# Kernel tuning notes

Hardware: AMD Instinct MI355X
Metric: run time of the kernel (lower is better)

Reference implementation:

```python
import jax, jax.numpy as jnp
import numpy as np

BN_EPS = 1e-5

def _conv(x, W, b, stride, pad):
    # x: [B,C,H,W], W: [O,I,kh,kw]
    y = jax.lax.conv_general_dilated(
        x, W, window_strides=(stride, stride),
        padding=[(pad, pad), (pad, pad)],
        dimension_numbers=('NCHW', 'OIHW', 'NCHW'))
    return y + b[None, :, None, None]

def _bn(x, gamma, beta, mean, var):
    inv = gamma * jax.lax.rsqrt(var + BN_EPS)
    return x * inv[None, :, None, None] + (beta - mean * inv)[None, :, None, None]

def _haar_cD(x):
    # pywt.dwt2(x, 'haar') diagonal detail over last two axes (even H,W):
    # cD[i,j] = (x[2i,2j] - x[2i,2j+1] - x[2i+1,2j] + x[2i+1,2j+1]) / 2
    a = x[..., 0::2, 0::2]
    b = x[..., 0::2, 1::2]
    c = x[..., 1::2, 0::2]
    d = x[..., 1::2, 1::2]
    return (a - b - c + d) * 0.5

def setup_inputs() -> dict:
    key = jax.random.key(0)
    ks = jax.random.split(key, 20)
    B = 8192
    f32 = jnp.float32
    inp = {
        'x':   jax.random.normal(ks[0], (B, 3, 32, 32), dtype=f32),
        # conv1: 3 -> 32, k5 s2 p2
        'w1':  jax.random.normal(ks[1], (32, 3, 5, 5), dtype=f32) * 0.05,
        'b1':  jnp.zeros((32,), f32),
        'g1':  jnp.ones((32,), f32),
        'be1': jnp.zeros((32,), f32),
        'm1':  jax.random.normal(ks[2], (32,), dtype=f32) * 0.1,
        'v1':  jax.random.uniform(ks[3], (32,), dtype=f32, minval=0.5, maxval=1.5),
        # conv2: 32 -> 64, k3 s2 p1
        'w2':  jax.random.normal(ks[4], (64, 32, 3, 3), dtype=f32) * 0.05,
        'b2':  jnp.zeros((64,), f32),
        'g2':  jnp.ones((64,), f32),
        'be2': jnp.zeros((64,), f32),
        'm2':  jax.random.normal(ks[5], (64,), dtype=f32) * 0.1,
        'v2':  jax.random.uniform(ks[6], (64,), dtype=f32, minval=0.5, maxval=1.5),
        # attention conv: 64 -> 1, k1
        'wa':  jax.random.normal(ks[7], (1, 64, 1, 1), dtype=f32) * 0.1,
        'ba':  jnp.zeros((1,), f32),
        # decoder linears (torch Linear layout: [out, in])
        'wd1': jax.random.normal(ks[8], (512, 64 * 8 * 8), dtype=f32) * 0.02,
        'bd1': jnp.zeros((512,), f32),
        'wd2': jax.random.normal(ks[9], (128, 512), dtype=f32) * 0.04,
        'bd2': jnp.zeros((128,), f32),
    }
    return inp

def reference(x, w1, b1, g1, be1, m1, v1, w2, b2, g2, be2, m2, v2,
              wa, ba, wd1, bd1, wd2, bd2):
    # wavelet_conv stem
    h = jax.nn.relu(_bn(_conv(x, w1, b1, 2, 2), g1, be1, m1, v1))   # [B,32,16,16]
    feat = jax.nn.relu(_bn(_conv(h, w2, b2, 2, 1), g2, be2, m2, v2))  # [B,64,8,8]
    # Haar DWT diagonal-detail gate (detached in the original)
    cD = jax.lax.stop_gradient(_haar_cD(feat))                        # [B,64,4,4]
    cD_up = jnp.repeat(jnp.repeat(cD, 2, axis=-2), 2, axis=-1)        # [B,64,8,8]
    feat = feat * cD_up
    # attention gate
    attn = jax.nn.sigmoid(_conv(feat, wa, ba, 1, 0))                  # [B,1,8,8]
    feat = feat * attn
    # decode
    f = feat.reshape(feat.shape[0], -1)                               # [B,4096]
    h1 = jax.nn.relu(f @ wd1.T + bd1)                                  # [B,512]
    return jax.nn.sigmoid(h1 @ wd2.T + bd2)                            # [B,128]
```

## Files before the change

### kernel.cpp

```cpp
#include <hip/hip_runtime.h>
#include <hip/hip_bf16.h>

typedef __bf16 bf16x8 __attribute__((ext_vector_type(8)));
typedef __bf16 bf16x4 __attribute__((ext_vector_type(4)));
typedef float f32x4 __attribute__((ext_vector_type(4)));

#define BN_EPS 1e-5f

__device__ __forceinline__ void gl_lds16(const __bf16* g, __bf16* l) {
    __builtin_amdgcn_global_load_lds(
        (const __attribute__((address_space(1))) unsigned int*)g,
        (__attribute__((address_space(3))) unsigned int*)l,
        16, 0, 0);
}

__global__ __launch_bounds__(256) void wd1p_kernel(const float* __restrict__ wd1, __bf16* __restrict__ o) {
    __shared__ float t2[64][65];
    const int n = blockIdx.x;
    const int tid = threadIdx.x;
    const float* src = wd1 + (size_t)n * 4096;
    #pragma unroll
    for (int r = 0; r < 16; ++r) {
        int j = r * 256 + tid;
        t2[j & 63][j >> 6] = src[j];
    }
    __syncthreads();
    __bf16* dst = o + (size_t)n * 4096;
    #pragma unroll
    for (int r = 0; r < 16; ++r) {
        int t = r * 256 + tid;
        dst[t] = (__bf16)t2[t >> 6][t & 63];
    }
}

__global__ void prep_kernel(const float* __restrict__ wd2, const float* __restrict__ w1,
                            const float* __restrict__ w2,
                            __bf16* __restrict__ wd2o, __bf16* __restrict__ w1o,
                            __bf16* __restrict__ w2o) {
    int i = blockIdx.x * 256 + threadIdx.x;
    if (i < 65536) { wd2o[i] = (__bf16)wd2[i]; return; }
    i -= 65536;
    if (i < 4096) {
        int oc = i >> 7, rem = i & 127;
        int ot = rem >> 3, j = rem & 7;
        float v = 0.f;
        if (ot < 15 && j < 5) {
            int ic = ot / 5, ky = ot % 5;
            v = w1[((oc * 3 + ic) * 5 + ky) * 5 + j];
        }
        w1o[i] = (__bf16)v;
        return;
    }
    i -= 4096;
    if (i < 18432) {
        int oc = i / 288, rem = i % 288;
        int tap = rem / 32, ic = rem % 32;
        w2o[i] = (__bf16)w2[(oc * 32 + ic) * 9 + tap];
    }
}

__global__ __launch_bounds__(256, 5) void conv_fused_kernel(
    const float* __restrict__ x,
    const __bf16* __restrict__ w1r, const float* __restrict__ b1,
    const float* __restrict__ g1, const float* __restrict__ be1,
    const float* __restrict__ m1, const float* __restrict__ v1,
    const __bf16* __restrict__ w2r, const float* __restrict__ b2,
    const float* __restrict__ g2, const float* __restrict__ be2,
    const float* __restrict__ m2, const float* __restrict__ v2,
    const float* __restrict__ wa, const float* __restrict__ ba,
    __bf16* __restrict__ f)
{
    __shared__ __align__(16) __bf16 xsb[3 * 36 * 40];
    __shared__ __align__(16) char  ubuf[23552];
    __bf16* hsf  = (__bf16*)ubuf;
    float*  feat = (float*)ubuf;
    float*  cds  = (float*)(ubuf + 17408);
    float*  atn  = (float*)(ubuf + 22528);

    const int b    = blockIdx.x;
    const int tid  = threadIdx.x;
    const int lane = tid & 63;
    const int wave = tid >> 6;
    const int lo   = lane >> 4;
    const int ln   = lane & 15;

    {
        bf16x8 z = {};
        for (int i = tid; i < 540; i += 256) *(bf16x8*)&xsb[i * 8] = z;
        if (tid < 132) {
            int pi = tid >> 2, ch = tid & 3;
            int pix = (pi < 17) ? pi : (pi - 16) * 17;
            *(bf16x8*)&hsf[pix * 40 + ch * 8] = z;
        }
    }
    __syncthreads();

    {
        const float4* xb = (const float4*)(x + (size_t)b * 3072);
        #pragma unroll
        for (int r = 0; r < 3; ++r) {
            int c = r * 256 + tid;
            int plane = c >> 8, rem = c & 255;
            int row = rem >> 3, c4 = rem & 7;
            float4 v = xb[c];
            bf16x4 h;
            h[0] = (__bf16)v.x; h[1] = (__bf16)v.y; h[2] = (__bf16)v.z; h[3] = (__bf16)v.w;
            *(bf16x4*)&xsb[plane * 1440 + (row + 2) * 40 + 4 + c4 * 4] = h;
        }
    }

    bf16x8 bw1[2][4];
    #pragma unroll
    for (int nt = 0; nt < 2; ++nt)
        #pragma unroll
        for (int s = 0; s < 4; ++s)
            bw1[nt][s] = *(const bf16x8*)(w1r + (nt * 16 + ln) * 128 + (s * 4 + lo) * 8);
    __syncthreads();

    f32x4 c1[4][2] = {};
    const unsigned int* xw = (const unsigned int*)xsb;
    #pragma unroll
    for (int s = 0; s < 4; ++s) {
        const int o  = s * 4 + lo;
        const int ic = (o * 205) >> 10;
        const int ky = o - ic * 5;
        const bool dummy = (o == 15);
        const int icc = dummy ? 2 : ic;
        #pragma unroll
        for (int mt = 0; mt < 4; ++mt) {
            const int oy  = wave * 4 + mt;
            const int row = dummy ? 35 : (2 * oy + ky);
            const int dw  = icc * 720 + row * 20 + ln + 1;
            union { unsigned int u[4]; bf16x8 v; } fa;
            fa.u[0] = xw[dw]; fa.u[1] = xw[dw + 1]; fa.u[2] = xw[dw + 2]; fa.u[3] = 0;
            #pragma unroll
            for (int nt = 0; nt < 2; ++nt)
                c1[mt][nt] = __builtin_amdgcn_mfma_f32_16x16x32_bf16(fa.v, bw1[nt][s], c1[mt][nt], 0, 0, 0);
        }
    }

    #pragma unroll
    for (int nt = 0; nt < 2; ++nt) {
        const int oc  = nt * 16 + ln;
        const float inv = g1[oc] * rsqrtf(v1[oc] + BN_EPS);
        const float bb  = be1[oc] + (b1[oc] - m1[oc]) * inv;
        #pragma unroll
        for (int mt = 0; mt < 4; ++mt) {
            const int hy = wave * 4 + mt + 1;
            #pragma unroll
            for (int r = 0; r < 4; ++r) {
                const int hx = lo * 4 + r + 1;
                hsf[(hy * 17 + hx) * 40 + oc] = (__bf16)fmaxf(c1[mt][nt][r] * inv + bb, 0.f);
            }
        }
    }

    const int wm = wave >> 1, wn = wave & 1;
    bf16x8 bw2[2][9];
    #pragma unroll
    for (int nt = 0; nt < 2; ++nt) {
        const __bf16* wp = w2r + (wn * 32 + nt * 16 + ln) * 288 + lo * 8;
        #pragma unroll
        for (int ks = 0; ks < 9; ++ks)
            bw2[nt][ks] = *(const bf16x8*)(wp + ks * 32);
    }
    __syncthreads();

    f32x4 c2[2][2] = {};
    {
        int pixbase[2];
        #pragma unroll
        for (int mt = 0; mt < 2; ++mt) {
            int p = wm * 32 + mt * 16 + ln;
            int qy = p >> 3, qx = p & 7;
            pixbase[mt] = (2 * qy * 17 + 2 * qx) * 40 + lo * 8;
        }
        #pragma unroll
        for (int ks = 0; ks < 9; ++ks) {
            const int ty = ks / 3, tx = ks % 3;
            bf16x8 af[2];
            #pragma unroll
            for (int mt = 0; mt < 2; ++mt)
                af[mt] = *(const bf16x8*)&hsf[pixbase[mt] + (ty * 17 + tx) * 40];
            #pragma unroll
            for (int mt = 0; mt < 2; ++mt)
                #pragma unroll
                for (int nt = 0; nt < 2; ++nt)
                    c2[mt][nt] = __builtin_amdgcn_mfma_f32_16x16x32_bf16(af[mt], bw2[nt][ks], c2[mt][nt], 0, 0, 0);
        }
    }
    __syncthreads();

    #pragma unroll
    for (int nt = 0; nt < 2; ++nt) {
        const int oc  = wn * 32 + nt * 16 + ln;
        const float inv = g2[oc] * rsqrtf(v2[oc] + BN_EPS);
        const float bb  = be2[oc] + (b2[oc] - m2[oc]) * inv;
        #pragma unroll
        for (int mt = 0; mt < 2; ++mt) {
            const int p0 = wm * 32 + mt * 16 + lo * 4;
            f32x4 o;
            #pragma unroll
            for (int r = 0; r < 4; ++r)
                o[r] = fmaxf(c2[mt][nt][r] * inv + bb, 0.f);
            *(f32x4*)&feat[oc * 68 + p0] = o;
        }
    }
    __syncthreads();

    {
        const int c = tid >> 2, y = tid & 3;
        const float* fr = feat + c * 68 + 16 * y;
        f32x4 t0 = *(const f32x4*)(fr);
        f32x4 t2 = *(const f32x4*)(fr + 4);
        f32x4 t1 = *(const f32x4*)(fr + 8);
        f32x4 t3 = *(const f32x4*)(fr + 12);
        f32x4 o;
        o[0] = 0.5f * (t0[0] - t0[1] - t1[0] + t1[1]);
        o[1] = 0.5f * (t0[2] - t0[3] - t1[2] + t1[3]);
        o[2] = 0.5f * (t2[0] - t2[1] - t3[0] + t3[1]);
        o[3] = 0.5f * (t2[2] - t2[3] - t3[2] + t3[3]);
        *(f32x4*)&cds[c * 20 + y * 4] = o;
    }
    __syncthreads();

    const int q  = tid & 63;
    const int g  = wave;
    const int qy2 = q >> 3, qx2 = q & 7;
    const int qq = (qy2 >> 1) * 4 + (qx2 >> 1);
    float a2[16];
    float part = 0.f;
    #pragma unroll
    for (int j = 0; j < 16; ++j) {
        int oc = g * 16 + j;
        float v = feat[oc * 68 + q] * cds[oc * 20 + qq];
        a2[j] = v;
        part += v * wa[oc];
    }
    atn[g * 64 + q] = part;
    __syncthreads();
    float s2  = atn[q] + atn[64 + q] + atn[128 + q] + atn[192 + q] + ba[0];
    float sig = 1.f / (1.f + __expf(-s2));

    bf16x8 fo0, fo1;
    #pragma unroll
    for (int j = 0; j < 8; ++j) {
        fo0[j] = (__bf16)(a2[j] * sig);
        fo1[j] = (__bf16)(a2[j + 8] * sig);
    }
    __bf16* fb = f + (size_t)b * 4096 + q * 64 + g * 16;
    *(bf16x8*)fb = fo0;
    *(bf16x8*)(fb + 8) = fo1;
}

__global__ __launch_bounds__(256, 4) void gemm1_split_kernel(
    const __bf16* __restrict__ A, const __bf16* __restrict__ B,
    float* __restrict__ P)
{
    const int K = 4096, NOUT = 512, KH = 2048;
    __shared__ __align__(16) __bf16 As[64][64];
    __shared__ __align__(16) __bf16 Bs[128][64];
    const int tid  = threadIdx.x;
    const int lane = tid & 63;
    const int wave = tid >> 6;
    const int lo = lane >> 4, ln = lane & 15;
    const int bid = blockIdx.x;
    const int swz = (bid & 7) * 128 + (bid >> 3);
    const int n0  = (swz & 3) * 128;
    const int zz  = (swz >> 2) & 1;
    const int m0  = (swz >> 3) * 64;
    const int ks0 = zz * KH;
    const int sw = ln & 7;
    f32x4 acc[4][2] = {};
    for (int k0 = ks0; k0 < ks0 + KH; k0 += 64) {
        #pragma unroll
        for (int r = 0; r < 2; ++r) {
            int i = r * 256 + tid;
            int row = i >> 3, cs = i & 7;
            gl_lds16(A + (size_t)(m0 + row) * K + k0 + (cs ^ (row & 7)) * 8, &As[0][0] + i * 8);
        }
        #pragma unroll
        for (int r = 0; r < 4; ++r) {
            int i = r * 256 + tid;
            int row = i >> 3, cs = i & 7;
            gl_lds16(B + (size_t)(n0 + row) * K + k0 + (cs ^ (row & 7)) * 8, &Bs[0][0] + i * 8);
        }
        __syncthreads();
        #pragma unroll
        for (int s = 0; s < 2; ++s) {
            const int c = s * 4 + lo;
            const int slot = (c ^ sw) * 8;
            bf16x8 af[4], bfr[2];
            #pragma unroll
            for (int mt = 0; mt < 4; ++mt)
                af[mt] = *(const bf16x8*)(&As[mt * 16 + ln][slot]);
            #pragma unroll
            for (int nt = 0; nt < 2; ++nt)
                bfr[nt] = *(const bf16x8*)(&Bs[wave * 32 + nt * 16 + ln][slot]);
            #pragma unroll
            for (int mt = 0; mt < 4; ++mt)
                #pragma unroll
                for (int nt = 0; nt < 2; ++nt)
                    acc[mt][nt] = __builtin_amdgcn_mfma_f32_16x16x32_bf16(af[mt], bfr[nt], acc[mt][nt], 0, 0, 0);
        }
        __syncthreads();
    }
    float* Pp = P + (size_t)zz * 8192 * 512;
    #pragma unroll
    for (int mt = 0; mt < 4; ++mt)
        #pragma unroll
        for (int nt = 0; nt < 2; ++nt)
            #pragma unroll
            for (int r = 0; r < 4; ++r) {
                int m = m0 + mt * 16 + lo * 4 + r;
                int n = n0 + wave * 32 + nt * 16 + ln;
                Pp[(size_t)m * NOUT + n] = acc[mt][nt][r];
            }
}

__global__ __launch_bounds__(256) void reduce1_kernel(
    const float* __restrict__ P, const float* __restrict__ bias, __bf16* __restrict__ h1)
{
    const size_t HALF = (size_t)8192 * 512;
    size_t i4 = ((size_t)blockIdx.x * 256 + threadIdx.x) * 4;
    f32x4 p0 = *(const f32x4*)(P + i4);
    f32x4 p1 = *(const f32x4*)(P + HALF + i4);
    f32x4 bv = *(const f32x4*)(bias + (i4 & 511));
    bf16x4 o;
    #pragma unroll
    for (int j = 0; j < 4; ++j)
        o[j] = (__bf16)fmaxf(p0[j] + p1[j] + bv[j], 0.f);
    *(bf16x4*)(h1 + i4) = o;
}

__global__ __launch_bounds__(256) void gemm1_kernel(
    const __bf16* __restrict__ A, const __bf16* __restrict__ B,
    const float* __restrict__ bias, __bf16* __restrict__ C)
{
    const int K = 4096, NOUT = 512;
    __shared__ __align__(16) __bf16 As[64][64];
    __shared__ __align__(16) __bf16 Bs[128][64];
    const int tid  = threadIdx.x;
    const int lane = tid & 63;
    const int wave = tid >> 6;
    const int lo = lane >> 4, ln = lane & 15;
    const int bid = blockIdx.x;
    const int swz = (bid & 7) * 64 + (bid >> 3);
    const int n0  = (swz & 3) * 128;
    const int m0  = (swz >> 2) * 64;
    const int sw = ln & 7;
    f32x4 acc[4][2] = {};
    for (int k0 = 0; k0 < K; k0 += 64) {
        #pragma unroll
        for (int r = 0; r < 2; ++r) {
            int i = r * 256 + tid;
            int row = i >> 3, cs = i & 7;
            gl_lds16(A + (size_t)(m0 + row) * K + k0 + (cs ^ (row & 7)) * 8, &As[0][0] + i * 8);
        }
        #pragma unroll
        for (int r = 0; r < 4; ++r) {
            int i = r * 256 + tid;
            int row = i >> 3, cs = i & 7;
            gl_lds16(B + (size_t)(n0 + row) * K + k0 + (cs ^ (row & 7)) * 8, &Bs[0][0] + i * 8);
        }
        __syncthreads();
        #pragma unroll
        for (int s = 0; s < 2; ++s) {
            const int c = s * 4 + lo;
            const int slot = (c ^ sw) * 8;
            bf16x8 af[4], bfr[2];
            #pragma unroll
            for (int mt = 0; mt < 4; ++mt)
                af[mt] = *(const bf16x8*)(&As[mt * 16 + ln][slot]);
            #pragma unroll
            for (int nt = 0; nt < 2; ++nt)
                bfr[nt] = *(const bf16x8*)(&Bs[wave * 32 + nt * 16 + ln][slot]);
            #pragma unroll
            for (int mt = 0; mt < 4; ++mt)
                #pragma unroll
                for (int nt = 0; nt < 2; ++nt)
                    acc[mt][nt] = __builtin_amdgcn_mfma_f32_16x16x32_bf16(af[mt], bfr[nt], acc[mt][nt], 0, 0, 0);
        }
        __syncthreads();
    }
    #pragma unroll
    for (int mt = 0; mt < 4; ++mt)
        #pragma unroll
        for (int nt = 0; nt < 2; ++nt)
            #pragma unroll
            for (int r = 0; r < 4; ++r) {
                int m = m0 + mt * 16 + lo * 4 + r;
                int n = n0 + wave * 32 + nt * 16 + ln;
                float v = acc[mt][nt][r] + bias[n];
                C[(size_t)m * NOUT + n] = (__bf16)fmaxf(v, 0.f);
            }
}

__global__ __launch_bounds__(256, 4) void gemm2_kernel(
    const __bf16* __restrict__ A, const __bf16* __restrict__ B,
    const float* __restrict__ bias, float* __restrict__ Out)
{
    const int K = 512, NOUT = 128;
    __shared__ __align__(16) __bf16 As[32][64];
    __shared__ __align__(16) __bf16 Bs[128][64];
    const int tid  = threadIdx.x;
    const int lane = tid & 63;
    const int wave = tid >> 6;
    const int lo = lane >> 4, ln = lane & 15;
    const int m0 = blockIdx.x * 32;
    const int sw = ln & 7;
    f32x4 acc[2][2] = {};
    for (int k0 = 0; k0 < K; k0 += 64) {
        {
            int i = tid;
            int row = i >> 3, cs = i & 7;
            gl_lds16(A + (size_t)(m0 + row) * K + k0 + (cs ^ (row & 7)) * 8, &As[0][0] + i * 8);
        }
        #pragma unroll
        for (int r = 0; r < 4; ++r) {
            int i = r * 256 + tid;
            int row = i >> 3, cs = i & 7;
            gl_lds16(B + (size_t)row * K + k0 + (cs ^ (row & 7)) * 8, &Bs[0][0] + i * 8);
        }
        __syncthreads();
        #pragma unroll
        for (int s = 0; s < 2; ++s) {
            const int c = s * 4 + lo;
            const int slot = (c ^ sw) * 8;
            bf16x8 af[2], bfr[2];
            #pragma unroll
            for (int mt = 0; mt < 2; ++mt)
                af[mt] = *(const bf16x8*)(&As[mt * 16 + ln][slot]);
            #pragma unroll
            for (int nt = 0; nt < 2; ++nt)
                bfr[nt] = *(const bf16x8*)(&Bs[wave * 32 + nt * 16 + ln][slot]);
            #pragma unroll
            for (int mt = 0; mt < 2; ++mt)
                #pragma unroll
                for (int nt = 0; nt < 2; ++nt)
                    acc[mt][nt] = __builtin_amdgcn_mfma_f32_16x16x32_bf16(af[mt], bfr[nt], acc[mt][nt], 0, 0, 0);
        }
        __syncthreads();
    }
    #pragma unroll
    for (int mt = 0; mt < 2; ++mt)
        #pragma unroll
        for (int nt = 0; nt < 2; ++nt)
            #pragma unroll
            for (int r = 0; r < 4; ++r) {
                int m = m0 + mt * 16 + lo * 4 + r;
                int n = wave * 32 + nt * 16 + ln;
                float v = acc[mt][nt][r] + bias[n];
                Out[(size_t)m * NOUT + n] = 1.f / (1.f + __expf(-v));
            }
}

extern "C" void kernel_launch(void* const* d_in, const int* in_sizes, int n_in,
                              void* d_out, int out_size, void* d_ws, size_t ws_size,
                              hipStream_t stream)
{
    const float* x   = (const float*)d_in[0];
    const float* w1  = (const float*)d_in[1];
    const float* b1  = (const float*)d_in[2];
    const float* g1  = (const float*)d_in[3];
    const float* be1 = (const float*)d_in[4];
    const float* m1  = (const float*)d_in[5];
    const float* v1  = (const float*)d_in[6];
    const float* w2  = (const float*)d_in[7];
    const float* b2  = (const float*)d_in[8];
    const float* g2  = (const float*)d_in[9];
    const float* be2 = (const float*)d_in[10];
    const float* m2  = (const float*)d_in[11];
    const float* v2  = (const float*)d_in[12];
    const float* wa  = (const float*)d_in[13];
    const float* ba  = (const float*)d_in[14];
    const float* wd1 = (const float*)d_in[15];
    const float* bd1 = (const float*)d_in[16];
    const float* wd2 = (const float*)d_in[17];
    const float* bd2 = (const float*)d_in[18];

    char* ws = (char*)d_ws;
    const size_t SZ_F  = 67108864;
    const size_t SZ_P  = 33554432;
    const size_t SZ_H1 = 8388608;
    const bool use_split = ws_size >= (SZ_F + SZ_P + SZ_H1 + 4194304 + 131072 + 65536 + 8192);

    __bf16* f_bf = (__bf16*)ws;
    float*  P;
    __bf16* h1_bf;
    char* tail;
    if (use_split) {
        P      = (float*)(ws + SZ_F);
        h1_bf  = (__bf16*)(ws + SZ_F + SZ_P);
        tail   = ws + SZ_F + SZ_P + SZ_H1;
    } else {
        P      = nullptr;
        h1_bf  = (__bf16*)(ws + SZ_F);
        tail   = ws + SZ_F + SZ_H1;
    }
    __bf16* wd1_bf = (__bf16*)tail;
    __bf16* wd2_bf = (__bf16*)(tail + 4194304);
    __bf16* w2r_bf = (__bf16*)(tail + 4194304 + 131072);
    __bf16* w1r_bf = (__bf16*)(tail + 4194304 + 131072 + 65536);

    prep_kernel<<<344, 256, 0, stream>>>(wd2, w1, w2, wd2_bf, w1r_bf, w2r_bf);
    wd1p_kernel<<<512, 256, 0, stream>>>(wd1, wd1_bf);

    conv_fused_kernel<<<8192, 256, 0, stream>>>(x, w1r_bf, b1, g1, be1, m1, v1,
                                                w2r_bf, b2, g2, be2, m2, v2, wa, ba, f_bf);

    if (use_split) {
        gemm1_split_kernel<<<1024, 256, 0, stream>>>(f_bf, wd1_bf, P);
        reduce1_kernel<<<4096, 256, 0, stream>>>(P, bd1, h1_bf);
    } else {
        gemm1_kernel<<<512, 256, 0, stream>>>(f_bf, wd1_bf, bd1, h1_bf);
    }

    gemm2_kernel<<<256, 256, 0, stream>>>(h1_bf, wd2_bf, bd2, (float*)d_out);
}
```

Before: 308.1 us.

## Widen conv block to 512 threads and use 128x128 split-K gemm1 tiles

The fused conv kernel now runs 512 threads per image: each wave owns half as many rows and output channels, and weight fragments are loaded per step instead of held in registers. The aim is to cut register pressure and raise occupancy. The first linear layer's split-K gemm grows from a 64x128 to a 128x128 tile per block and can split K four ways when workspace allows, with the reduce kernel summing a variable number of partials. This brings more data reuse per block and more parallel blocks, at the cost of extra partial-sum traffic and lower gemm occupancy.

```diff
diff --git a/kernel.cpp b/kernel.cpp
--- a/kernel.cpp
+++ b/kernel.cpp
@@ -4,6 +4,7 @@
 typedef __bf16 bf16x8 __attribute__((ext_vector_type(8)));
 typedef __bf16 bf16x4 __attribute__((ext_vector_type(4)));
 typedef float f32x4 __attribute__((ext_vector_type(4)));
+typedef float f32x2 __attribute__((ext_vector_type(2)));
 
 #define BN_EPS 1e-5f
 
@@ -59,7 +60,7 @@
     }
 }
 
-__global__ __launch_bounds__(256, 5) void conv_fused_kernel(
+__global__ __launch_bounds__(512, 8) void conv_fused_kernel(
     const float* __restrict__ x,
     const __bf16* __restrict__ w1r, const float* __restrict__ b1,
     const float* __restrict__ g1, const float* __restrict__ be1,
@@ -71,7 +72,7 @@
     __bf16* __restrict__ f)
 {
     __shared__ __align__(16) __bf16 xsb[3 * 36 * 40];
-    __shared__ __align__(16) char  ubuf[23552];
+    __shared__ __align__(16) char  ubuf[24576];
     __bf16* hsf  = (__bf16*)ubuf;
     float*  feat = (float*)ubuf;
     float*  cds  = (float*)(ubuf + 17408);
@@ -86,7 +87,7 @@
 
     {
         bf16x8 z = {};
-        for (int i = tid; i < 540; i += 256) *(bf16x8*)&xsb[i * 8] = z;
+        for (int i = tid; i < 540; i += 512) *(bf16x8*)&xsb[i * 8] = z;
         if (tid < 132) {
             int pi = tid >> 2, ch = tid & 3;
             int pix = (pi < 17) ? pi : (pi - 16) * 17;
@@ -98,44 +99,43 @@
     {
         const float4* xb = (const float4*)(x + (size_t)b * 3072);
         #pragma unroll
-        for (int r = 0; r < 3; ++r) {
-            int c = r * 256 + tid;
-            int plane = c >> 8, rem = c & 255;
-            int row = rem >> 3, c4 = rem & 7;
-            float4 v = xb[c];
-            bf16x4 h;
-            h[0] = (__bf16)v.x; h[1] = (__bf16)v.y; h[2] = (__bf16)v.z; h[3] = (__bf16)v.w;
-            *(bf16x4*)&xsb[plane * 1440 + (row + 2) * 40 + 4 + c4 * 4] = h;
-        }
-    }
-
-    bf16x8 bw1[2][4];
-    #pragma unroll
-    for (int nt = 0; nt < 2; ++nt)
-        #pragma unroll
-        for (int s = 0; s < 4; ++s)
-            bw1[nt][s] = *(const bf16x8*)(w1r + (nt * 16 + ln) * 128 + (s * 4 + lo) * 8);
-    __syncthreads();
-
-    f32x4 c1[4][2] = {};
+        for (int r = 0; r < 2; ++r) {
+            int c = r * 512 + tid;
+            if (c < 768) {
+                int plane = c >> 8, rem = c & 255;
+                int row = rem >> 3, c4 = rem & 7;
+                float4 v = xb[c];
+                bf16x4 h;
+                h[0] = (__bf16)v.x; h[1] = (__bf16)v.y; h[2] = (__bf16)v.z; h[3] = (__bf16)v.w;
+                *(bf16x4*)&xsb[plane * 1440 + (row + 2) * 40 + 4 + c4 * 4] = h;
+            }
+        }
+    }
+    __syncthreads();
+
+    f32x4 c1[2][2] = {};
     const unsigned int* xw = (const unsigned int*)xsb;
-    #pragma unroll
+    #pragma unroll 1
     for (int s = 0; s < 4; ++s) {
+        bf16x8 bw1s[2];
+        #pragma unroll
+        for (int nt = 0; nt < 2; ++nt)
+            bw1s[nt] = *(const bf16x8*)(w1r + (nt * 16 + ln) * 128 + (s * 4 + lo) * 8);
         const int o  = s * 4 + lo;
         const int ic = (o * 205) >> 10;
         const int ky = o - ic * 5;
         const bool dummy = (o == 15);
         const int icc = dummy ? 2 : ic;
         #pragma unroll
-        for (int mt = 0; mt < 4; ++mt) {
-            const int oy  = wave * 4 + mt;
+        for (int mt = 0; mt < 2; ++mt) {
+            const int oy  = wave * 2 + mt;
             const int row = dummy ? 35 : (2 * oy + ky);
             const int dw  = icc * 720 + row * 20 + ln + 1;
             union { unsigned int u[4]; bf16x8 v; } fa;
             fa.u[0] = xw[dw]; fa.u[1] = xw[dw + 1]; fa.u[2] = xw[dw + 2]; fa.u[3] = 0;
             #pragma unroll
             for (int nt = 0; nt < 2; ++nt)
-                c1[mt][nt] = __builtin_amdgcn_mfma_f32_16x16x32_bf16(fa.v, bw1[nt][s], c1[mt][nt], 0, 0, 0);
+                c1[mt][nt] = __builtin_amdgcn_mfma_f32_16x16x32_bf16(fa.v, bw1s[nt], c1[mt][nt], 0, 0, 0);
         }
     }
 
@@ -145,8 +145,8 @@
         const float inv = g1[oc] * rsqrtf(v1[oc] + BN_EPS);
         const float bb  = be1[oc] + (b1[oc] - m1[oc]) * inv;
         #pragma unroll
-        for (int mt = 0; mt < 4; ++mt) {
-            const int hy = wave * 4 + mt + 1;
+        for (int mt = 0; mt < 2; ++mt) {
+            const int hy = wave * 2 + mt + 1;
             #pragma unroll
             for (int r = 0; r < 4; ++r) {
                 const int hx = lo * 4 + r + 1;
@@ -154,19 +154,10 @@
             }
         }
     }
-
-    const int wm = wave >> 1, wn = wave & 1;
-    bf16x8 bw2[2][9];
-    #pragma unroll
-    for (int nt = 0; nt < 2; ++nt) {
-        const __bf16* wp = w2r + (wn * 32 + nt * 16 + ln) * 288 + lo * 8;
-        #pragma unroll
-        for (int ks = 0; ks < 9; ++ks)
-            bw2[nt][ks] = *(const bf16x8*)(wp + ks * 32);
-    }
-    __syncthreads();
-
-    f32x4 c2[2][2] = {};
+    __syncthreads();
+
+    const int wm = wave >> 2, wn = wave & 3;
+    f32x4 c2[2] = {};
     {
         int pixbase[2];
         #pragma unroll
@@ -175,25 +166,23 @@
             int qy = p >> 3, qx = p & 7;
             pixbase[mt] = (2 * qy * 17 + 2 * qx) * 40 + lo * 8;
         }
-        #pragma unroll
+        const __bf16* wp = w2r + (wn * 16 + ln) * 288 + lo * 8;
+        #pragma unroll 1
         for (int ks = 0; ks < 9; ++ks) {
+            bf16x8 bw2s = *(const bf16x8*)(wp + ks * 32);
             const int ty = ks / 3, tx = ks % 3;
-            bf16x8 af[2];
-            #pragma unroll
-            for (int mt = 0; mt < 2; ++mt)
-                af[mt] = *(const bf16x8*)&hsf[pixbase[mt] + (ty * 17 + tx) * 40];
-            #pragma unroll
-            for (int mt = 0; mt < 2; ++mt)
-                #pragma unroll
-                for (int nt = 0; nt < 2; ++nt)
-                    c2[mt][nt] = __builtin_amdgcn_mfma_f32_16x16x32_bf16(af[mt], bw2[nt][ks], c2[mt][nt], 0, 0, 0);
-        }
-    }
-    __syncthreads();
-
-    #pragma unroll
-    for (int nt = 0; nt < 2; ++nt) {
-        const int oc  = wn * 32 + nt * 16 + ln;
+            const int off = (ty * 17 + tx) * 40;
+            #pragma unroll
+            for (int mt = 0; mt < 2; ++mt) {
+                bf16x8 af = *(const bf16x8*)&hsf[pixbase[mt] + off];
+                c2[mt] = __builtin_amdgcn_mfma_f32_16x16x32_bf16(af, bw2s, c2[mt], 0, 0, 0);
+            }
+        }
+    }
+    __syncthreads();
+
+    {
+        const int oc  = wn * 16 + ln;
         const float inv = g2[oc] * rsqrtf(v2[oc] + BN_EPS);
         const float bb  = be2[oc] + (b2[oc] - m2[oc]) * inv;
         #pragma unroll
@@ -202,79 +191,75 @@
             f32x4 o;
             #pragma unroll
             for (int r = 0; r < 4; ++r)
-                o[r] = fmaxf(c2[mt][nt][r] * inv + bb, 0.f);
+                o[r] = fmaxf(c2[mt][r] * inv + bb, 0.f);
             *(f32x4*)&feat[oc * 68 + p0] = o;
         }
     }
     __syncthreads();
 
     {
-        const int c = tid >> 2, y = tid & 3;
-        const float* fr = feat + c * 68 + 16 * y;
+        const int c = tid >> 3, y = (tid >> 1) & 3, h = tid & 1;
+        const float* fr = feat + c * 68 + 16 * y + 4 * h;
         f32x4 t0 = *(const f32x4*)(fr);
-        f32x4 t2 = *(const f32x4*)(fr + 4);
         f32x4 t1 = *(const f32x4*)(fr + 8);
-        f32x4 t3 = *(const f32x4*)(fr + 12);
-        f32x4 o;
+        f32x2 o;
         o[0] = 0.5f * (t0[0] - t0[1] - t1[0] + t1[1]);
         o[1] = 0.5f * (t0[2] - t0[3] - t1[2] + t1[3]);
-        o[2] = 0.5f * (t2[0] - t2[1] - t3[0] + t3[1]);
-        o[3] = 0.5f * (t2[2] - t2[3] - t3[2] + t3[3]);
-        *(f32x4*)&cds[c * 20 + y * 4] = o;
-    }
-    __syncthreads();
-
-    const int q  = tid & 63;
+        *(f32x2*)&cds[c * 20 + y * 4 + 2 * h] = o;
+    }
+    __syncthreads();
+
+    const int q  = lane;
     const int g  = wave;
     const int qy2 = q >> 3, qx2 = q & 7;
     const int qq = (qy2 >> 1) * 4 + (qx2 >> 1);
-    float a2[16];
+    float a2[8];
     float part = 0.f;
     #pragma unroll
-    for (int j = 0; j < 16; ++j) {
-        int oc = g * 16 + j;
+    for (int j = 0; j < 8; ++j) {
+        int oc = g * 8 + j;
         float v = feat[oc * 68 + q] * cds[oc * 20 + qq];
         a2[j] = v;
         part += v * wa[oc];
     }
     atn[g * 64 + q] = part;
     __syncthreads();
-    float s2  = atn[q] + atn[64 + q] + atn[128 + q] + atn[192 + q] + ba[0];
+    float s2 = ba[0];
+    #pragma unroll
+    for (int k = 0; k < 8; ++k) s2 += atn[k * 64 + q];
     float sig = 1.f / (1.f + __expf(-s2));
 
-    bf16x8 fo0, fo1;
-    #pragma unroll
-    for (int j = 0; j < 8; ++j) {
-        fo0[j] = (__bf16)(a2[j] * sig);
-        fo1[j] = (__bf16)(a2[j + 8] * sig);
-    }
-    __bf16* fb = f + (size_t)b * 4096 + q * 64 + g * 16;
-    *(bf16x8*)fb = fo0;
-    *(bf16x8*)(fb + 8) = fo1;
-}
-
-__global__ __launch_bounds__(256, 4) void gemm1_split_kernel(
+    bf16x8 fo;
+    #pragma unroll
+    for (int j = 0; j < 8; ++j)
+        fo[j] = (__bf16)(a2[j] * sig);
+    *(bf16x8*)(f + (size_t)b * 4096 + q * 64 + g * 8) = fo;
+}
+
+__global__ __launch_bounds__(256, 3) void gemm1_split_kernel(
     const __bf16* __restrict__ A, const __bf16* __restrict__ B,
-    float* __restrict__ P)
+    float* __restrict__ P, int zlog, int chunk)
 {
-    const int K = 4096, NOUT = 512, KH = 2048;
-    __shared__ __align__(16) __bf16 As[64][64];
+    const int K = 4096, NOUT = 512;
+    const int KH = K >> zlog;
+    __shared__ __align__(16) __bf16 As[128][64];
     __shared__ __align__(16) __bf16 Bs[128][64];
     const int tid  = threadIdx.x;
     const int lane = tid & 63;
     const int wave = tid >> 6;
     const int lo = lane >> 4, ln = lane & 15;
+    const int wm = wave >> 1, wn = wave & 1;
     const int bid = blockIdx.x;
-    const int swz = (bid & 7) * 128 + (bid >> 3);
+    const int swz = (bid & 7) * chunk + (bid >> 3);
     const int n0  = (swz & 3) * 128;
-    const int zz  = (swz >> 2) & 1;
-    const int m0  = (swz >> 3) * 64;
+    const int zz  = (swz >> 2) & ((1 << zlog) - 1);
+    const int m0  = (swz >> (2 + zlog)) * 128;
     const int ks0 = zz * KH;
-    const int sw = ln & 7;
-    f32x4 acc[4][2] = {};
+    const int sw  = ln & 7;
+    f32x4 acc[4][4] = {};
     for (int k0 = ks0; k0 < ks0 + KH; k0 += 64) {
         #pragma unroll
-        for (int r = 0; r < 2; ++r) {
+        for (int r = 0; r < 4; ++r) {
             int i = r * 256 + tid;
             int row = i >> 3, cs = i & 7;
             gl_lds16(A + (size_t)(m0 + row) * K + k0 + (cs ^ (row & 7)) * 8, &As[0][0] + i * 8);
@@ -290,17 +275,17 @@
         for (int s = 0; s < 2; ++s) {
             const int c = s * 4 + lo;
             const int slot = (c ^ sw) * 8;
-            bf16x8 af[4], bfr[2];
+            bf16x8 af[4], bfr[4];
             #pragma unroll
             for (int mt = 0; mt < 4; ++mt)
-                af[mt] = *(const bf16x8*)(&As[mt * 16 + ln][slot]);
-            #pragma unroll
-            for (int nt = 0; nt < 2; ++nt)
-                bfr[nt] = *(const bf16x8*)(&Bs[wave * 32 + nt * 16 + ln][slot]);
+                af[mt] = *(const bf16x8*)(&As[wm * 64 + mt * 16 + ln][slot]);
+            #pragma unroll
+            for (int nt = 0; nt < 4; ++nt)
+                bfr[nt] = *(const bf16x8*)(&Bs[wn * 64 + nt * 16 + ln][slot]);
             #pragma unroll
             for (int mt = 0; mt < 4; ++mt)
                 #pragma unroll
-                for (int nt = 0; nt < 2; ++nt)
+                for (int nt = 0; nt < 4; ++nt)
                     acc[mt][nt] = __builtin_amdgcn_mfma_f32_16x16x32_bf16(af[mt], bfr[nt], acc[mt][nt], 0, 0, 0);
         }
         __syncthreads();
@@ -309,27 +294,29 @@
     #pragma unroll
     for (int mt = 0; mt < 4; ++mt)
         #pragma unroll
-        for (int nt = 0; nt < 2; ++nt)
+        for (int nt = 0; nt < 4; ++nt)
             #pragma unroll
             for (int r = 0; r < 4; ++r) {
-                int m = m0 + mt * 16 + lo * 4 + r;
-                int n = n0 + wave * 32 + nt * 16 + ln;
+                int m = m0 + wm * 64 + mt * 16 + lo * 4 + r;
+                int n = n0 + wn * 64 + nt * 16 + ln;
                 Pp[(size_t)m * NOUT + n] = acc[mt][nt][r];
             }
 }
 
 __global__ __launch_bounds__(256) void reduce1_kernel(
-    const float* __restrict__ P, const float* __restrict__ bias, __bf16* __restrict__ h1)
+    const float* __restrict__ P, const float* __restrict__ bias, __bf16* __restrict__ h1,
+    int nz)
 {
-    const size_t HALF = (size_t)8192 * 512;
+    const size_t Q = (size_t)8192 * 512;
     size_t i4 = ((size_t)blockIdx.x * 256 + threadIdx.x) * 4;
-    f32x4 p0 = *(const f32x4*)(P + i4);
-    f32x4 p1 = *(const f32x4*)(P + HALF + i4);
+    f32x4 s = *(const f32x4*)(P + i4);
+    for (int z = 1; z < nz; ++z)
+        s += *(const f32x4*)(P + (size_t)z * Q + i4);
     f32x4 bv = *(const f32x4*)(bias + (i4 & 511));
     bf16x4 o;
     #pragma unroll
     for (int j = 0; j < 4; ++j)
-        o[j] = (__bf16)fmaxf(p0[j] + p1[j] + bv[j], 0.f);
+        o[j] = (__bf16)fmaxf(s[j] + bv[j], 0.f);
     *(bf16x4*)(h1 + i4) = o;
 }
 
@@ -480,16 +467,21 @@
     const float* bd2 = (const float*)d_in[18];
 
     char* ws = (char*)d_ws;
-    const size_t SZ_F  = 67108864;
-    const size_t SZ_P  = 33554432;
-    const size_t SZ_H1 = 8388608;
-    const bool use_split = ws_size >= (SZ_F + SZ_P + SZ_H1 + 4194304 + 131072 + 65536 + 8192);
+    const size_t SZ_F   = 67108864;
+    const size_t SZ_H1  = 8388608;
+    const size_t SZ_P1  = 16777216;
+    const size_t TAILSZ = 4194304 + 131072 + 65536 + 8192;
+
+    int nz = 0;
+    if      (ws_size >= SZ_F + 4 * SZ_P1 + SZ_H1 + TAILSZ) nz = 4;
+    else if (ws_size >= SZ_F + 2 * SZ_P1 + SZ_H1 + TAILSZ) nz = 2;
 
     __bf16* f_bf = (__bf16*)ws;
     float*  P;
     __bf16* h1_bf;
     char* tail;
-    if (use_split) {
+    if (nz) {
+        size_t SZ_P = (size_t)nz * SZ_P1;
         P      = (float*)(ws + SZ_F);
         h1_bf  = (__bf16*)(ws + SZ_F + SZ_P);
         tail   = ws + SZ_F + SZ_P + SZ_H1;
@@ -506,12 +498,14 @@
     prep_kernel<<<344, 256, 0, stream>>>(wd2, w1, w2, wd2_bf, w1r_bf, w2r_bf);
     wd1p_kernel<<<512, 256, 0, stream>>>(wd1, wd1_bf);
 
-    conv_fused_kernel<<<8192, 256, 0, stream>>>(x, w1r_bf, b1, g1, be1, m1, v1,
+    conv_fused_kernel<<<8192, 512, 0, stream>>>(x, w1r_bf, b1, g1, be1, m1, v1,
                                                 w2r_bf, b2, g2, be2, m2, v2, wa, ba, f_bf);
 
-    if (use_split) {
-        gemm1_split_kernel<<<1024, 256, 0, stream>>>(f_bf, wd1_bf, P);
-        reduce1_kernel<<<4096, 256, 0, stream>>>(P, bd1, h1_bf);
+    if (nz) {
+        const int zlog = (nz == 4) ? 2 : 1;
+        const int blocks = 256 * nz;
+        gemm1_split_kernel<<<blocks, 256, 0, stream>>>(f_bf, wd1_bf, P, zlog, blocks >> 3);
+        reduce1_kernel<<<4096, 256, 0, stream>>>(P, bd1, h1_bf, nz);
     } else {
         gemm1_kernel<<<512, 256, 0, stream>>>(f_bf, wd1_bf, bd1, h1_bf);
     }
```

Measured after the change: 353.8 us. +14.8%, slower.

## Fuse split-K reduction into gemm2 and process two images per conv block

Applied to the files above, without the earlier changes.

Removes the separate reduce1 kernel: when split-K is used, gemm2 loads both fp32 partial sums, adds the bias, applies ReLU and converts to bf16 directly into its LDS A tile. This drops one launch and the h1 write/read round trip. The conv kernel now runs 512-thread blocks that each handle two images with duplicated shared buffers, which halves the number of blocks. The trade-offs are a synchronous load path in place of async global_load_lds, and a different occupancy profile with 2 blocks per CU.

```diff
diff --git a/kernel.cpp b/kernel.cpp
--- a/kernel.cpp
+++ b/kernel.cpp
@@ -59,7 +59,7 @@
     }
 }
 
-__global__ __launch_bounds__(256, 5) void conv_fused_kernel(
+__global__ __launch_bounds__(512, 2) void conv_fused_kernel(
     const float* __restrict__ x,
     const __bf16* __restrict__ w1r, const float* __restrict__ b1,
     const float* __restrict__ g1, const float* __restrict__ be1,
@@ -70,25 +70,30 @@
     const float* __restrict__ wa, const float* __restrict__ ba,
     __bf16* __restrict__ f)
 {
-    __shared__ __align__(16) __bf16 xsb[3 * 36 * 40];
-    __shared__ __align__(16) char  ubuf[23552];
+    __shared__ __align__(16) __bf16 xsb2[2][3 * 36 * 40];
+    __shared__ __align__(16) char  ubuf2[2][23552];
+
+    const int tid  = threadIdx.x;
+    const int half = tid >> 8;
+    const int t    = tid & 255;
+    __bf16* xsb  = xsb2[half];
+    char*   ubuf = ubuf2[half];
     __bf16* hsf  = (__bf16*)ubuf;
     float*  feat = (float*)ubuf;
     float*  cds  = (float*)(ubuf + 17408);
     float*  atn  = (float*)(ubuf + 22528);
 
-    const int b    = blockIdx.x;
-    const int tid  = threadIdx.x;
-    const int lane = tid & 63;
-    const int wave = tid >> 6;
+    const int b    = blockIdx.x * 2 + half;
+    const int lane = t & 63;
+    const int wave = t >> 6;
     const int lo   = lane >> 4;
     const int ln   = lane & 15;
 
     {
         bf16x8 z = {};
-        for (int i = tid; i < 540; i += 256) *(bf16x8*)&xsb[i * 8] = z;
-        if (tid < 132) {
-            int pi = tid >> 2, ch = tid & 3;
+        for (int i = t; i < 540; i += 256) *(bf16x8*)&xsb[i * 8] = z;
+        if (t < 132) {
+            int pi = t >> 2, ch = t & 3;
             int pix = (pi < 17) ? pi : (pi - 16) * 17;
             *(bf16x8*)&hsf[pix * 40 + ch * 8] = z;
         }
@@ -99,7 +104,7 @@
         const float4* xb = (const float4*)(x + (size_t)b * 3072);
         #pragma unroll
         for (int r = 0; r < 3; ++r) {
-            int c = r * 256 + tid;
+            int c = r * 256 + t;
             int plane = c >> 8, rem = c & 255;
             int row = rem >> 3, c4 = rem & 7;
             float4 v = xb[c];
@@ -209,22 +214,22 @@
     __syncthreads();
 
     {
-        const int c = tid >> 2, y = tid & 3;
+        const int c = t >> 2, y = t & 3;
         const float* fr = feat + c * 68 + 16 * y;
         f32x4 t0 = *(const f32x4*)(fr);
-        f32x4 t2 = *(const f32x4*)(fr + 4);
+        f32x4 t2v = *(const f32x4*)(fr + 4);
         f32x4 t1 = *(const f32x4*)(fr + 8);
         f32x4 t3 = *(const f32x4*)(fr + 12);
         f32x4 o;
         o[0] = 0.5f * (t0[0] - t0[1] - t1[0] + t1[1]);
         o[1] = 0.5f * (t0[2] - t0[3] - t1[2] + t1[3]);
-        o[2] = 0.5f * (t2[0] - t2[1] - t3[0] + t3[1]);
-        o[3] = 0.5f * (t2[2] - t2[3] - t3[2] + t3[3]);
+        o[2] = 0.5f * (t2v[0] - t2v[1] - t3[0] + t3[1]);
+        o[3] = 0.5f * (t2v[2] - t2v[3] - t3[2] + t3[3]);
         *(f32x4*)&cds[c * 20 + y * 4] = o;
     }
     __syncthreads();
 
-    const int q  = tid & 63;
+    const int q  = t & 63;
     const int g  = wave;
     const int qy2 = q >> 3, qx2 = q & 7;
     const int qq = (qy2 >> 1) * 4 + (qx2 >> 1);
@@ -318,21 +323,6 @@
             }
 }
 
-__global__ __launch_bounds__(256) void reduce1_kernel(
-    const float* __restrict__ P, const float* __restrict__ bias, __bf16* __restrict__ h1)
-{
-    const size_t HALF = (size_t)8192 * 512;
-    size_t i4 = ((size_t)blockIdx.x * 256 + threadIdx.x) * 4;
-    f32x4 p0 = *(const f32x4*)(P + i4);
-    f32x4 p1 = *(const f32x4*)(P + HALF + i4);
-    f32x4 bv = *(const f32x4*)(bias + (i4 & 511));
-    bf16x4 o;
-    #pragma unroll
-    for (int j = 0; j < 4; ++j)
-        o[j] = (__bf16)fmaxf(p0[j] + p1[j] + bv[j], 0.f);
-    *(bf16x4*)(h1 + i4) = o;
-}
-
 __global__ __launch_bounds__(256) void gemm1_kernel(
     const __bf16* __restrict__ A, const __bf16* __restrict__ B,
     const float* __restrict__ bias, __bf16* __restrict__ C)
@@ -397,8 +387,9 @@
 }
 
 __global__ __launch_bounds__(256, 4) void gemm2_kernel(
-    const __bf16* __restrict__ A, const __bf16* __restrict__ B,
-    const float* __restrict__ bias, float* __restrict__ Out)
+    const __bf16* __restrict__ A, const float* __restrict__ P,
+    const float* __restrict__ bd1, const __bf16* __restrict__ B,
+    const float* __restrict__ bias, float* __restrict__ Out, int fused)
 {
     const int K = 512, NOUT = 128;
     __shared__ __align__(16) __bf16 As[32][64];
@@ -409,12 +400,31 @@
     const int lo = lane >> 4, ln = lane & 15;
     const int m0 = blockIdx.x * 32;
     const int sw = ln & 7;
+    const size_t HALF = (size_t)8192 * 512;
     f32x4 acc[2][2] = {};
     for (int k0 = 0; k0 < K; k0 += 64) {
         {
             int i = tid;
             int row = i >> 3, cs = i & 7;
-            gl_lds16(A + (size_t)(m0 + row) * K + k0 + (cs ^ (row & 7)) * 8, &As[0][0] + i * 8);
+            int k = k0 + (cs ^ (row & 7)) * 8;
+            if (fused) {
+                const float* p0 = P + (size_t)(m0 + row) * K + k;
+                f32x4 a0 = *(const f32x4*)(p0);
+                f32x4 a1 = *(const f32x4*)(p0 + 4);
+                f32x4 c0 = *(const f32x4*)(p0 + HALF);
+                f32x4 c1 = *(const f32x4*)(p0 + HALF + 4);
+                f32x4 b0 = *(const f32x4*)(bd1 + k);
+                f32x4 b1v = *(const f32x4*)(bd1 + k + 4);
+                bf16x8 o;
+                #pragma unroll
+                for (int j = 0; j < 4; ++j) {
+                    o[j]     = (__bf16)fmaxf(a0[j] + c0[j] + b0[j], 0.f);
+                    o[j + 4] = (__bf16)fmaxf(a1[j] + c1[j] + b1v[j], 0.f);
+                }
+                *(bf16x8*)(&As[0][0] + i * 8) = o;
+            } else {
+                gl_lds16(A + (size_t)(m0 + row) * K + k, &As[0][0] + i * 8);
+            }
         }
         #pragma unroll
         for (int r = 0; r < 4; ++r) {
@@ -506,15 +516,14 @@
     prep_kernel<<<344, 256, 0, stream>>>(wd2, w1, w2, wd2_bf, w1r_bf, w2r_bf);
     wd1p_kernel<<<512, 256, 0, stream>>>(wd1, wd1_bf);
 
-    conv_fused_kernel<<<8192, 256, 0, stream>>>(x, w1r_bf, b1, g1, be1, m1, v1,
+    conv_fused_kernel<<<4096, 512, 0, stream>>>(x, w1r_bf, b1, g1, be1, m1, v1,
                                                 w2r_bf, b2, g2, be2, m2, v2, wa, ba, f_bf);
 
     if (use_split) {
         gemm1_split_kernel<<<1024, 256, 0, stream>>>(f_bf, wd1_bf, P);
-        reduce1_kernel<<<4096, 256, 0, stream>>>(P, bd1, h1_bf);
+        gemm2_kernel<<<256, 256, 0, stream>>>(nullptr, P, bd1, wd2_bf, bd2, (float*)d_out, 1);
     } else {
         gemm1_kernel<<<512, 256, 0, stream>>>(f_bf, wd1_bf, bd1, h1_bf);
-    }
-
-    gemm2_kernel<<<256, 256, 0, stream>>>(h1_bf, wd2_bf, bd2, (float*)d_out);
-}
+        gemm2_kernel<<<256, 256, 0, stream>>>(h1_bf, nullptr, bd1, wd2_bf, bd2, (float*)d_out, 0);
+    }
+}
```

After: 311.2 us. No clear change (+1.0%).
